# Optimization experiments

Measured on AMD Instinct MI355X. Metric: run time of the kernel, lower is better.

Reference implementation:

```python
import jax, jax.numpy as jnp
import numpy as np

EPS = 1e-12  # matches torch F.normalize default eps
TEMP = 0.1


def _gram(x):
    # L2-normalize rows; for unit vectors 1 - 0.5*||xi-xj||^2 == xi . xj
    n = x / jnp.maximum(jnp.linalg.norm(x, axis=-1, keepdims=True), EPS)
    return n @ n.T  # [N, N]


def setup_inputs() -> dict:
    key = jax.random.key(0)
    k1, k2, k3, k4 = jax.random.split(key, 4)
    N, D = 4096, 512
    return {
        "fm_rgb": jax.random.normal(k1, (N, D), dtype=jnp.float32),
        "fm_depth": jax.random.normal(k2, (N, D), dtype=jnp.float32),
        "fm_ir": jax.random.normal(k3, (N, D), dtype=jnp.float32),
        "fm_t": jax.random.normal(k4, (N, D), dtype=jnp.float32),
    }


def reference(fm_rgb, fm_depth, fm_ir, fm_t):
    G_rgb = _gram(fm_rgb)
    G_depth = _gram(fm_depth)
    G_ir = _gram(fm_ir)
    G_t = _gram(fm_t)
    inv_t = 1.0 / TEMP
    loss_rgb = jnp.mean((G_t * inv_t - G_rgb * inv_t) ** 2)
    loss_depth = jnp.mean((G_t * inv_t - G_depth * inv_t) ** 2)
    loss_ir = jnp.mean((G_t * inv_t - G_ir * inv_t) ** 2)
    return loss_rgb + loss_depth + loss_ir
```

## Files before the change

### kernel.cpp

```cpp
#include <hip/hip_runtime.h>
#include <hip/hip_bf16.h>


typedef __attribute__((ext_vector_type(4))) float floatx4;
typedef __attribute__((ext_vector_type(8))) unsigned short ushort8;
typedef __attribute__((ext_vector_type(2))) long long llx2;

#define N_ROWS 4096
#define DDIM   512
#define LOSS_SCALE 9.094947017729282e-11f

__device__ __forceinline__ const float* sel_mod(int mod, const float* a,
                                                const float* b, const float* c,
                                                const float* d) {
  return mod == 0 ? a : mod == 1 ? b : mod == 2 ? c : d;
}

__global__ __launch_bounds__(256) void preprocess_kernel(
    const float* __restrict__ in0, const float* __restrict__ in1,
    const float* __restrict__ in2, const float* __restrict__ in3,
    unsigned char* __restrict__ nT8, float* __restrict__ out) {
  int mod = blockIdx.y;
  int k0 = blockIdx.x * 64;
  const float* X = sel_mod(mod, in0, in1, in2, in3) + (size_t)k0 * DDIM;

  if (blockIdx.x == 0 && blockIdx.y == 0 && threadIdx.x == 0)
    out[0] = 0.f;

  __shared__ float rsc[64];
  __shared__ unsigned short tile[128][72];

  int t = threadIdx.x;
  int w = t >> 6, lane = t & 63;

#pragma unroll
  for (int i = 0; i < 16; ++i) {
    int r = w * 16 + i;
    const float4* rp = (const float4*)(X + (size_t)r * DDIM);
    float4 a = rp[lane];
    float4 b = rp[lane + 64];
    float ss = a.x * a.x + a.y * a.y + a.z * a.z + a.w * a.w +
               b.x * b.x + b.y * b.y + b.z * b.z + b.w * b.w;
#pragma unroll
    for (int off = 32; off > 0; off >>= 1) ss += __shfl_down(ss, off, 64);
    if (lane == 0) rsc[r] = 16.0f / fmaxf(sqrtf(ss), 1e-12f);
  }
  __syncthreads();

  for (int p = 0; p < 4; ++p) {
#pragma unroll
    for (int it = 0; it < 8; ++it) {
      int idx = it * 256 + t;
      int r = idx >> 5;
      int c4 = idx & 31;
      float4 v = ((const float4*)(X + (size_t)r * DDIM + p * 128))[c4];
      float sc = rsc[r];
      __hip_bfloat16 h0 = __float2bfloat16(v.x * sc);
      __hip_bfloat16 h1 = __float2bfloat16(v.y * sc);
      __hip_bfloat16 h2 = __float2bfloat16(v.z * sc);
      __hip_bfloat16 h3 = __float2bfloat16(v.w * sc);
      tile[c4 * 4 + 0][r] = *(unsigned short*)&h0;
      tile[c4 * 4 + 1][r] = *(unsigned short*)&h1;
      tile[c4 * 4 + 2][r] = *(unsigned short*)&h2;
      tile[c4 * 4 + 3][r] = *(unsigned short*)&h3;
    }
    __syncthreads();
#pragma unroll
    for (int it = 0; it < 2; ++it) {
      int idx = it * 256 + t;
      int c = idx >> 2;
      int g = idx & 3;
      ushort8 u0 = *(const ushort8*)&tile[c][g * 16];
      ushort8 u1 = *(const ushort8*)&tile[c][g * 16 + 8];
      float f[16];
#pragma unroll
      for (int j = 0; j < 8; ++j) {
        f[j] = __uint_as_float(((unsigned int)(unsigned short)u0[j]) << 16);
        f[8 + j] = __uint_as_float(((unsigned int)(unsigned short)u1[j]) << 16);
      }
      unsigned int wds[4];
#pragma unroll
      for (int q = 0; q < 4; ++q) {
        unsigned int pk =
            __builtin_amdgcn_cvt_pk_fp8_f32(f[4 * q], f[4 * q + 1], 0, 0);
        pk = __builtin_amdgcn_cvt_pk_fp8_f32(f[4 * q + 2], f[4 * q + 3], pk, 1);
        wds[q] = pk;
      }
      uint4 o = {wds[0], wds[1], wds[2], wds[3]};
      *(uint4*)(nT8 + ((size_t)(mod * DDIM + p * 128 + c)) * N_ROWS + k0 +
                g * 16) = o;
    }
    __syncthreads();
  }
}

__device__ __forceinline__ void stage_tiles(
    const unsigned char* __restrict__ Abase,
    const unsigned char* __restrict__ Bbase, int k0,
    unsigned char* ls, int w, int lane) {
  int rr = lane >> 3;
  int s = lane & 7;
#pragma unroll
  for (int c = 0; c < 2; ++c) {
    int base = c * 32 + w * 8;
    int row = base + rr;
    int gc = s ^ ((row >> 1) & 7);
    const unsigned char* ga = Abase + (size_t)row * N_ROWS + k0 + gc * 16;
    __builtin_amdgcn_global_load_lds(
        (__attribute__((address_space(1))) void*)(void*)ga,
        (__attribute__((address_space(3))) void*)(void*)&ls[base * 128],
        16, 0, 0);
  }
#pragma unroll
  for (int c = 0; c < 2; ++c) {
    int base = c * 32 + w * 8;
    int row = base + rr;
    int gc = s ^ ((row >> 1) & 7);
    const unsigned char* gb = Bbase + (size_t)row * N_ROWS + k0 + gc * 16;
    __builtin_amdgcn_global_load_lds(
        (__attribute__((address_space(1))) void*)(void*)gb,
        (__attribute__((address_space(3))) void*)(void*)&ls[8192 + base * 128],
        16, 0, 0);
  }
}

__device__ __forceinline__ void compute_tiles(
    const unsigned char* ls, floatx4 acc[2][2], int wm, int wn, int lm,
    int lq) {
  llx2 A16[2][2], B16[2][2];
#pragma unroll
  for (int mi = 0; mi < 2; ++mi) {
    int row = wm + mi * 16 + lm;
    int sw = (row >> 1) & 7;
    A16[mi][0] = *(const llx2*)&ls[row * 128 + ((lq * 2) ^ sw) * 16];
    A16[mi][1] = *(const llx2*)&ls[row * 128 + ((lq * 2 + 1) ^ sw) * 16];
  }
#pragma unroll
  for (int ni = 0; ni < 2; ++ni) {
    int row = wn + ni * 16 + lm;
    int sw = (row >> 1) & 7;
    B16[ni][0] = *(const llx2*)&ls[8192 + row * 128 + ((lq * 2) ^ sw) * 16];
    B16[ni][1] =
        *(const llx2*)&ls[8192 + row * 128 + ((lq * 2 + 1) ^ sw) * 16];
  }
#pragma unroll
  for (int ks = 0; ks < 4; ++ks) {
    int h = ks >> 1, e = ks & 1;
#pragma unroll
    for (int mi = 0; mi < 2; ++mi)
#pragma unroll
      for (int ni = 0; ni < 2; ++ni)
        acc[mi][ni] = __builtin_amdgcn_mfma_f32_16x16x32_fp8_fp8(
            A16[mi][h][e], B16[ni][h][e], acc[mi][ni], 0, 0, 0);
  }
}

__global__ __launch_bounds__(256) void gram_frob_kernel(
    const unsigned char* __restrict__ nT8, float* __restrict__ out) {
  __shared__ __align__(16) unsigned char ls[2][16384];
  __shared__ float red[4];

  const int   pa[7] = {3, 0, 1, 2, 3, 3, 3};
  const int   pb[7] = {3, 0, 1, 2, 0, 1, 2};
  const float pw[7] = {3.f, 1.f, 1.f, 1.f, -2.f, -2.f, -2.f};

  int prod = blockIdx.y;
  int a0 = (blockIdx.x >> 3) * 64;
  int b0 = (blockIdx.x & 7) * 64;
  const unsigned char* Abase = nT8 + ((size_t)pa[prod] * DDIM + a0) * N_ROWS;
  const unsigned char* Bbase = nT8 + ((size_t)pb[prod] * DDIM + b0) * N_ROWS;

  int t = threadIdx.x;
  int w = t >> 6;
  int lane = t & 63;
  int wm = (w >> 1) * 32;
  int wn = (w & 1) * 32;
  int lm = lane & 15;
  int lq = lane >> 4;

  floatx4 zero = {0.f, 0.f, 0.f, 0.f};
  floatx4 acc[2][2];
#pragma unroll
  for (int mi = 0; mi < 2; ++mi)
#pragma unroll
    for (int ni = 0; ni < 2; ++ni) acc[mi][ni] = zero;

  stage_tiles(Abase, Bbase, 0, ls[0], w, lane);
  __syncthreads();
  for (int i = 0; i < 15; ++i) {
    int k0 = (2 * i + 1) * 128;
    stage_tiles(Abase, Bbase, k0, ls[1], w, lane);
    compute_tiles(ls[0], acc, wm, wn, lm, lq);
    __syncthreads();
    stage_tiles(Abase, Bbase, k0 + 128, ls[0], w, lane);
    compute_tiles(ls[1], acc, wm, wn, lm, lq);
    __syncthreads();
  }
  stage_tiles(Abase, Bbase, 31 * 128, ls[1], w, lane);
  compute_tiles(ls[0], acc, wm, wn, lm, lq);
  __syncthreads();
  compute_tiles(ls[1], acc, wm, wn, lm, lq);

  float s = 0.f;
#pragma unroll
  for (int mi = 0; mi < 2; ++mi)
#pragma unroll
    for (int ni = 0; ni < 2; ++ni)
#pragma unroll
      for (int r = 0; r < 4; ++r) {
        float v = acc[mi][ni][r];
        s += v * v;
      }
#pragma unroll
  for (int off = 32; off > 0; off >>= 1) s += __shfl_down(s, off, 64);
  if (lane == 0) red[w] = s;
  __syncthreads();
  if (t == 0) {
    float tot = red[0] + red[1] + red[2] + red[3];
    atomicAdd(out, pw[prod] * LOSS_SCALE * tot);
  }
}

extern "C" void kernel_launch(void* const* d_in, const int* in_sizes, int n_in,
                              void* d_out, int out_size, void* d_ws, size_t ws_size,
                              hipStream_t stream) {
  const float* in_rgb   = (const float*)d_in[0];
  const float* in_depth = (const float*)d_in[1];
  const float* in_ir    = (const float*)d_in[2];
  const float* in_t     = (const float*)d_in[3];

  unsigned char* nT8 = (unsigned char*)d_ws;

  preprocess_kernel<<<dim3(64, 4), 256, 0, stream>>>(
      in_rgb, in_depth, in_ir, in_t, nT8, (float*)d_out);
  gram_frob_kernel<<<dim3(64, 7), 256, 0, stream>>>(nT8, (float*)d_out);
}
```

Measured before the change: 119.1 us.

## Exploit Gram symmetry for self-products and restructure fp8 preprocess transpose

The 512x512 self-product Frobenius blocks now compute only upper-triangular tiles, with off-diagonal tiles weighted by two. This cuts the four symmetric products from 64 tiles to 36 each, giving 336 blocks instead of 448. The preprocess kernel now handles 32 rows per block (twice as many blocks) and converts to fp8 before transposing through a smaller padded LDS buffer. The bf16 rounding step is kept so the numerics should stay the same.

```diff
diff --git a/kernel.cpp b/kernel.cpp
--- a/kernel.cpp
+++ b/kernel.cpp
@@ -3,7 +3,6 @@
 
 
 typedef __attribute__((ext_vector_type(4))) float floatx4;
-typedef __attribute__((ext_vector_type(8))) unsigned short ushort8;
 typedef __attribute__((ext_vector_type(2))) long long llx2;
 
 #define N_ROWS 4096
@@ -14,6 +13,12 @@
                                                 const float* b, const float* c,
                                                 const float* d) {
   return mod == 0 ? a : mod == 1 ? b : mod == 2 ? c : d;
+}
+
+__device__ __forceinline__ float bfr(float x) {
+  __hip_bfloat16 h = __float2bfloat16(x);
+  unsigned short u = *(unsigned short*)&h;
+  return __uint_as_float(((unsigned int)u) << 16);
 }
 
 __global__ __launch_bounds__(256) void preprocess_kernel(
@@ -21,21 +26,21 @@
     const float* __restrict__ in2, const float* __restrict__ in3,
     unsigned char* __restrict__ nT8, float* __restrict__ out) {
   int mod = blockIdx.y;
-  int k0 = blockIdx.x * 64;
+  int k0 = blockIdx.x * 32;
   const float* X = sel_mod(mod, in0, in1, in2, in3) + (size_t)k0 * DDIM;
 
   if (blockIdx.x == 0 && blockIdx.y == 0 && threadIdx.x == 0)
     out[0] = 0.f;
 
-  __shared__ float rsc[64];
-  __shared__ unsigned short tile[128][72];
+  __shared__ float rsc[32];
+  __shared__ unsigned int t8[128 * 9];
 
   int t = threadIdx.x;
   int w = t >> 6, lane = t & 63;
 
 #pragma unroll
-  for (int i = 0; i < 16; ++i) {
-    int r = w * 16 + i;
+  for (int i = 0; i < 8; ++i) {
+    int r = w * 8 + i;
     const float4* rp = (const float4*)(X + (size_t)r * DDIM);
     float4 a = rp[lane];
     float4 b = rp[lane + 64];
@@ -47,47 +52,36 @@
   }
   __syncthreads();
 
+  int ag = t >> 5;
+  int bg = t & 31;
+  float sc[4];
+#pragma unroll
+  for (int q = 0; q < 4; ++q) sc[q] = rsc[ag * 4 + q];
+
   for (int p = 0; p < 4; ++p) {
-#pragma unroll
-    for (int it = 0; it < 8; ++it) {
-      int idx = it * 256 + t;
-      int r = idx >> 5;
-      int c4 = idx & 31;
-      float4 v = ((const float4*)(X + (size_t)r * DDIM + p * 128))[c4];
-      float sc = rsc[r];
-      __hip_bfloat16 h0 = __float2bfloat16(v.x * sc);
-      __hip_bfloat16 h1 = __float2bfloat16(v.y * sc);
-      __hip_bfloat16 h2 = __float2bfloat16(v.z * sc);
-      __hip_bfloat16 h3 = __float2bfloat16(v.w * sc);
-      tile[c4 * 4 + 0][r] = *(unsigned short*)&h0;
-      tile[c4 * 4 + 1][r] = *(unsigned short*)&h1;
-      tile[c4 * 4 + 2][r] = *(unsigned short*)&h2;
-      tile[c4 * 4 + 3][r] = *(unsigned short*)&h3;
+    float4 v[4];
+#pragma unroll
+    for (int q = 0; q < 4; ++q)
+      v[q] = ((const float4*)(X + (size_t)(ag * 4 + q) * DDIM + p * 128))[bg];
+#pragma unroll
+    for (int j = 0; j < 4; ++j) {
+      float f0 = bfr(((const float*)&v[0])[j] * sc[0]);
+      float f1 = bfr(((const float*)&v[1])[j] * sc[1]);
+      float f2 = bfr(((const float*)&v[2])[j] * sc[2]);
+      float f3 = bfr(((const float*)&v[3])[j] * sc[3]);
+      unsigned int pk = __builtin_amdgcn_cvt_pk_fp8_f32(f0, f1, 0, 0);
+      pk = __builtin_amdgcn_cvt_pk_fp8_f32(f2, f3, pk, 1);
+      t8[(bg * 4 + j) * 9 + ag] = pk;
     }
     __syncthreads();
-#pragma unroll
-    for (int it = 0; it < 2; ++it) {
-      int idx = it * 256 + t;
-      int c = idx >> 2;
-      int g = idx & 3;
-      ushort8 u0 = *(const ushort8*)&tile[c][g * 16];
-      ushort8 u1 = *(const ushort8*)&tile[c][g * 16 + 8];
-      float f[16];
-#pragma unroll
-      for (int j = 0; j < 8; ++j) {
-        f[j] = __uint_as_float(((unsigned int)(unsigned short)u0[j]) << 16);
-        f[8 + j] = __uint_as_float(((unsigned int)(unsigned short)u1[j]) << 16);
-      }
-      unsigned int wds[4];
-#pragma unroll
-      for (int q = 0; q < 4; ++q) {
-        unsigned int pk =
-            __builtin_amdgcn_cvt_pk_fp8_f32(f[4 * q], f[4 * q + 1], 0, 0);
-        pk = __builtin_amdgcn_cvt_pk_fp8_f32(f[4 * q + 2], f[4 * q + 3], pk, 1);
-        wds[q] = pk;
-      }
-      uint4 o = {wds[0], wds[1], wds[2], wds[3]};
-      *(uint4*)(nT8 + ((size_t)(mod * DDIM + p * 128 + c)) * N_ROWS + k0 +
+    {
+      int col = t >> 1, g = t & 1;
+      uint4 o;
+      o.x = t8[col * 9 + g * 4 + 0];
+      o.y = t8[col * 9 + g * 4 + 1];
+      o.z = t8[col * 9 + g * 4 + 2];
+      o.w = t8[col * 9 + g * 4 + 3];
+      *(uint4*)(nT8 + ((size_t)(mod * DDIM + p * 128 + col)) * N_ROWS + k0 +
                 g * 16) = o;
     }
     __syncthreads();
@@ -160,15 +154,36 @@
   __shared__ __align__(16) unsigned char ls[2][16384];
   __shared__ float red[4];
 
-  const int   pa[7] = {3, 0, 1, 2, 3, 3, 3};
-  const int   pb[7] = {3, 0, 1, 2, 0, 1, 2};
-  const float pw[7] = {3.f, 1.f, 1.f, 1.f, -2.f, -2.f, -2.f};
-
-  int prod = blockIdx.y;
-  int a0 = (blockIdx.x >> 3) * 64;
-  int b0 = (blockIdx.x & 7) * 64;
-  const unsigned char* Abase = nT8 + ((size_t)pa[prod] * DDIM + a0) * N_ROWS;
-  const unsigned char* Bbase = nT8 + ((size_t)pb[prod] * DDIM + b0) * N_ROWS;
+  int bx = blockIdx.x;
+  int pa_, pb_, ti, tj;
+  float wgt;
+  if (bx < 144) {
+    int p = bx / 36;
+    int t36 = bx - p * 36;
+    int i = 0;
+    while (t36 >= 8 - i) { t36 -= 8 - i; ++i; }
+    ti = i;
+    tj = i + t36;
+    const int   sm[4] = {3, 0, 1, 2};
+    const float sw_[4] = {3.f, 1.f, 1.f, 1.f};
+    pa_ = sm[p];
+    pb_ = sm[p];
+    wgt = sw_[p] * (ti == tj ? 1.f : 2.f);
+  } else {
+    int r = bx - 144;
+    int p = r >> 6;
+    int t64 = r & 63;
+    ti = t64 >> 3;
+    tj = t64 & 7;
+    pa_ = 3;
+    pb_ = p;
+    wgt = -2.f;
+  }
+
+  int a0 = ti * 64;
+  int b0 = tj * 64;
+  const unsigned char* Abase = nT8 + ((size_t)pa_ * DDIM + a0) * N_ROWS;
+  const unsigned char* Bbase = nT8 + ((size_t)pb_ * DDIM + b0) * N_ROWS;
 
   int t = threadIdx.x;
   int w = t >> 6;
@@ -217,7 +232,7 @@
   __syncthreads();
   if (t == 0) {
     float tot = red[0] + red[1] + red[2] + red[3];
-    atomicAdd(out, pw[prod] * LOSS_SCALE * tot);
+    atomicAdd(out, wgt * LOSS_SCALE * tot);
   }
 }
 
@@ -231,7 +246,7 @@
 
   unsigned char* nT8 = (unsigned char*)d_ws;
 
-  preprocess_kernel<<<dim3(64, 4), 256, 0, stream>>>(
+  preprocess_kernel<<<dim3(128, 4), 256, 0, stream>>>(
       in_rgb, in_depth, in_ir, in_t, nT8, (float*)d_out);
-  gram_frob_kernel<<<dim3(64, 7), 256, 0, stream>>>(nT8, (float*)d_out);
-}
+  gram_frob_kernel<<<dim3(336), 256, 0, stream>>>(nT8, (float*)d_out);
+}
```

After: 109.9 us. 1.08x faster.
